# Kernel tuning notes

Measured on AMD Instinct MI355X. Metric: run time of the kernel, lower is better.

Reference implementation:

```python
import jax, jax.numpy as jnp
import numpy as np

N_NODES = 50000
N_EDGES = 800000
IN_DIM = 128
HID = 64
N_GRAPHS = 256


def gcn_conv(x, W, b, src, dst, num_nodes):
    """PyG GCNConv: add self-loops, sym norm D^-1/2 (A+I) D^-1/2, linear, bias."""
    h = x @ W  # [N, out]
    loop = jnp.arange(num_nodes)
    s = jnp.concatenate([src, loop])
    d = jnp.concatenate([dst, loop])
    ones = jnp.ones(d.shape, h.dtype)
    deg = jax.ops.segment_sum(ones, d, num_segments=num_nodes)
    dinv = jnp.where(deg > 0, jax.lax.rsqrt(deg), 0.0)
    norm = dinv[s] * dinv[d]  # [E+N]
    msg = h[s] * norm[:, None]  # gather + scale (memory bound)
    out = jax.ops.segment_sum(msg, d, num_segments=num_nodes)  # scatter-add
    return out + b


def setup_inputs() -> dict:
    key = jax.random.key(0)
    ks = jax.random.split(key, 8)
    x = jax.random.normal(ks[0], (N_NODES, IN_DIM), dtype=jnp.float32)
    edge_index = jax.random.randint(ks[1], (2, N_EDGES), 0, N_NODES, dtype=jnp.int64)
    batch = jnp.sort(jax.random.randint(ks[2], (N_NODES,), 0, N_GRAPHS, dtype=jnp.int64))
    W1 = jax.random.normal(ks[3], (IN_DIM, HID), dtype=jnp.float32) / np.sqrt(IN_DIM)
    b1 = jnp.zeros((HID,), jnp.float32)
    W2 = jax.random.normal(ks[4], (HID, HID), dtype=jnp.float32) / np.sqrt(HID)
    b2 = jnp.zeros((HID,), jnp.float32)
    Wl = jax.random.normal(ks[5], (HID, 1), dtype=jnp.float32) / np.sqrt(HID)
    bl = jnp.zeros((1,), jnp.float32)
    return {"x": x, "W1": W1, "b1": b1, "W2": W2, "b2": b2,
            "Wl": Wl, "bl": bl, "edge_index": edge_index, "batch": batch}


def reference(x, W1, b1, W2, b2, Wl, bl, edge_index, batch):
    n = x.shape[0]
    src, dst = edge_index[0], edge_index[1]
    h = jax.nn.relu(gcn_conv(x, W1, b1, src, dst, n))
    # dropout is identity in eval mode
    h = jax.nn.relu(gcn_conv(h, W2, b2, src, dst, n))
    ones = jnp.ones((n,), h.dtype)
    counts = jax.ops.segment_sum(ones, batch, num_segments=N_GRAPHS)
    pooled = jax.ops.segment_sum(h, batch, num_segments=N_GRAPHS)
    pooled = pooled / jnp.maximum(counts, 1.0)[:, None]  # global_mean_pool
    return (pooled @ Wl + bl).reshape(-1)  # [N_GRAPHS]
```

## Files before the change

kernel.cpp:

```cpp
#include <hip/hip_runtime.h>
#include <hip/hip_fp16.h>
#include <math.h>

__global__ void zero32(int* __restrict__ p, int n) {
    int i = blockIdx.x * blockDim.x + threadIdx.x;
    if (i < n) p[i] = 0;
}

__global__ void hist_rank(const int* __restrict__ dst, int* __restrict__ cnt,
                          unsigned short* __restrict__ rank, int E) {
    int e = blockIdx.x * blockDim.x + threadIdx.x;
    if (e < E) rank[e] = (unsigned short)atomicAdd(&cnt[dst[e]], 1);
}

__global__ __launch_bounds__(256) void scan1_dinv(const int* __restrict__ cnt,
                                                  int* __restrict__ excl,
                                                  int* __restrict__ sums,
                                                  float* __restrict__ dinv, int n) {
    int i = blockIdx.x * 256 + threadIdx.x;
    int v = (i < n) ? cnt[i] : 0;
    if (i < n) dinv[i] = rsqrtf((float)(v + 1));
    int lane = threadIdx.x & 63;
    int w = threadIdx.x >> 6;
    int s = v;
#pragma unroll
    for (int off = 1; off < 64; off <<= 1) {
        int t = __shfl_up(s, off, 64);
        if (lane >= off) s += t;
    }
    __shared__ int wsum[4];
    if (lane == 63) wsum[w] = s;
    __syncthreads();
    int woff = 0;
#pragma unroll
    for (int k = 0; k < 3; ++k) if (k < w) woff += wsum[k];
    int incl = s + woff;
    if (i < n) excl[i] = incl - v;
    if (threadIdx.x == 255) sums[blockIdx.x] = incl;
}

__global__ __launch_bounds__(256) void scan2(int* __restrict__ sums, int nb) {
    int t = threadIdx.x;
    int v = (t < nb) ? sums[t] : 0;
    int lane = t & 63;
    int w = t >> 6;
    int s = v;
#pragma unroll
    for (int off = 1; off < 64; off <<= 1) {
        int u = __shfl_up(s, off, 64);
        if (lane >= off) s += u;
    }
    __shared__ int wsum[4];
    if (lane == 63) wsum[w] = s;
    __syncthreads();
    int woff = 0;
#pragma unroll
    for (int k = 0; k < 3; ++k) if (k < w) woff += wsum[k];
    int incl = s + woff;
    if (t < nb) sums[t] = incl - v;
}

__global__ __launch_bounds__(256) void scan3(const int* __restrict__ excl,
                                             const int* __restrict__ sums,
                                             int* __restrict__ rowptr, int n, int E) {
    int i = blockIdx.x * 256 + threadIdx.x;
    if (i < n) rowptr[i] = excl[i] + sums[i >> 8];
    if (i == n) rowptr[n] = E;
}

__global__ void fill_place(const int* __restrict__ src, const int* __restrict__ dst,
                           const unsigned short* __restrict__ rank,
                           const int* __restrict__ rowptr,
                           unsigned short* __restrict__ col, int E, int n) {
    const int g    = blockIdx.x & 7;
    const int nblk = gridDim.x >> 3;
    const int bid  = blockIdx.x >> 3;
    const int lo = (int)(((long)g * n) >> 3);
    const int hi = (int)(((long)(g + 1) * n) >> 3);
    for (long e = (long)bid * blockDim.x + threadIdx.x; e < E;
         e += (long)nblk * blockDim.x) {
        int d = dst[e];
        if (d < lo || d >= hi) continue;
        col[rowptr[d] + rank[e]] = (unsigned short)src[e];
    }
}

#define RL(x, k) __int_as_float(__builtin_amdgcn_readlane(__float_as_int(x), (k)))

__device__ __forceinline__ float ldf(const float* p, long i) { return p[i]; }
__device__ __forceinline__ float ldf(const __half* p, long i) { return __half2float(p[i]); }
__device__ __forceinline__ void stf(float* p, long i, float v) { p[i] = v; }
__device__ __forceinline__ void stf(__half* p, long i, float v) { p[i] = __float2half(v); }

template <int K, typename XT, typename YT>
__global__ __launch_bounds__(256) void gemm_bcast_scaled(const XT* __restrict__ X,
                                                         const float* __restrict__ W,
                                                         const float* __restrict__ dinv,
                                                         YT* __restrict__ Y, int n) {
    const int lane = threadIdx.x & 63;
    const long wid = (((long)blockIdx.x * blockDim.x) + threadIdx.x) >> 6;
    const long nw  = ((long)gridDim.x * blockDim.x) >> 6;

    float wr[K];
#pragma unroll
    for (int k = 0; k < K; ++k) wr[k] = W[k * 64 + lane];
#pragma unroll
    for (int k = 0; k < K; ++k) asm volatile("" : "+v"(wr[k]));

    long r0 = wid;
    if (r0 >= n) return;
    float xa0 = ldf(X, r0 * K + lane);
    float xb0 = 0.f;
    if constexpr (K > 64) xb0 = ldf(X, r0 * K + 64 + lane);
    float dv0 = dinv[r0];

    long r1 = r0 + nw;
    bool h1 = r1 < n;
    long rc1 = h1 ? r1 : r0;
    float xa1 = ldf(X, rc1 * K + lane);
    float xb1 = 0.f;
    if constexpr (K > 64) xb1 = ldf(X, rc1 * K + 64 + lane);
    float dv1 = dinv[rc1];

    while (true) {
        long r2 = r1 + nw;
        bool h2 = h1 && (r2 < n);
        long rc2 = h2 ? r2 : r0;
        float xa2 = ldf(X, rc2 * K + lane);
        float xb2 = 0.f;
        if constexpr (K > 64) xb2 = ldf(X, rc2 * K + 64 + lane);
        float dv2 = dinv[rc2];

        float a0 = 0.f, a1 = 0.f, a2 = 0.f, a3 = 0.f;
#pragma unroll
        for (int k = 0; k < 64; k += 4) {
            a0 = fmaf(RL(xa0, k + 0), wr[k + 0], a0);
            a1 = fmaf(RL(xa0, k + 1), wr[k + 1], a1);
            a2 = fmaf(RL(xa0, k + 2), wr[k + 2], a2);
            a3 = fmaf(RL(xa0, k + 3), wr[k + 3], a3);
        }
        if constexpr (K > 64) {
#pragma unroll
            for (int k = 0; k < 64; k += 4) {
                a0 = fmaf(RL(xb0, k + 0), wr[64 + k + 0], a0);
                a1 = fmaf(RL(xb0, k + 1), wr[64 + k + 1], a1);
                a2 = fmaf(RL(xb0, k + 2), wr[64 + k + 2], a2);
                a3 = fmaf(RL(xb0, k + 3), wr[64 + k + 3], a3);
            }
        }
        stf(Y, r0 * 64 + lane, dv0 * ((a0 + a1) + (a2 + a3)));
        if (!h1) break;
        r0 = r1; xa0 = xa1; xb0 = xb1; dv0 = dv1;
        r1 = r2; h1 = h2; xa1 = xa2; xb1 = xb2; dv1 = dv2;
    }
}

#define HG(idx) ldf(Hp, (long)(idx) * 64 + j)
template <typename HT>
__device__ __forceinline__ void agg2(const HT* __restrict__ Hp,
                                     const int* __restrict__ rowptr,
                                     const unsigned short* __restrict__ col,
                                     long vA, long vB, int j, bool hasB,
                                     float& sumA, float& sumB) {
    float a0 = HG(vA), a1 = 0.f, a2 = 0.f, a3 = 0.f;
    float b0 = 0.f, b1 = 0.f, b2 = 0.f, b3 = 0.f;
    int pA = rowptr[vA], pA1 = rowptr[vA + 1];
    int pB = 0, pB1 = 0;
    if (hasB) { b0 = HG(vB); pB = rowptr[vB]; pB1 = rowptr[vB + 1]; }
    if ((pA & 1) && pA < pA1) { a1 += HG(col[pA]); ++pA; }
    if ((pB & 1) && pB < pB1) { b1 += HG(col[pB]); ++pB; }
    unsigned int cA01 = *(const unsigned int*)(col + pA);
    unsigned int cA23 = *(const unsigned int*)(col + pA + 2);
    unsigned int cB01 = *(const unsigned int*)(col + pB);
    unsigned int cB23 = *(const unsigned int*)(col + pB + 2);
    while (pA + 4 <= pA1 && pB + 4 <= pB1) {
        unsigned int nA01 = *(const unsigned int*)(col + pA + 4);
        unsigned int nA23 = *(const unsigned int*)(col + pA + 6);
        unsigned int nB01 = *(const unsigned int*)(col + pB + 4);
        unsigned int nB23 = *(const unsigned int*)(col + pB + 6);
        float hA0 = HG(cA01 & 0xFFFFu);
        float hA1 = HG(cA01 >> 16);
        float hA2 = HG(cA23 & 0xFFFFu);
        float hA3 = HG(cA23 >> 16);
        float hB0 = HG(cB01 & 0xFFFFu);
        float hB1 = HG(cB01 >> 16);
        float hB2 = HG(cB23 & 0xFFFFu);
        float hB3 = HG(cB23 >> 16);
        a0 += hA0; a1 += hA1; a2 += hA2; a3 += hA3;
        b0 += hB0; b1 += hB1; b2 += hB2; b3 += hB3;
        cA01 = nA01; cA23 = nA23; cB01 = nB01; cB23 = nB23;
        pA += 4; pB += 4;
    }
    for (; pA + 4 <= pA1; pA += 4) {
        float h0 = HG(cA01 & 0xFFFFu);
        float h1 = HG(cA01 >> 16);
        float h2 = HG(cA23 & 0xFFFFu);
        float h3 = HG(cA23 >> 16);
        a0 += h0; a1 += h1; a2 += h2; a3 += h3;
        cA01 = *(const unsigned int*)(col + pA + 4);
        cA23 = *(const unsigned int*)(col + pA + 6);
    }
    for (; pA < pA1; ++pA) a1 += HG(col[pA]);
    for (; pB + 4 <= pB1; pB += 4) {
        float h0 = HG(cB01 & 0xFFFFu);
        float h1 = HG(cB01 >> 16);
        float h2 = HG(cB23 & 0xFFFFu);
        float h3 = HG(cB23 >> 16);
        b0 += h0; b1 += h1; b2 += h2; b3 += h3;
        cB01 = *(const unsigned int*)(col + pB + 4);
        cB23 = *(const unsigned int*)(col + pB + 6);
    }
    for (; pB < pB1; ++pB) b1 += HG(col[pB]);
    sumA = (a0 + a1) + (a2 + a3);
    sumB = (b0 + b1) + (b2 + b3);
}

__global__ __launch_bounds__(256) void agg_relu(const __half* __restrict__ Hp,
                                                const int* __restrict__ rowptr,
                                                const unsigned short* __restrict__ col,
                                                const float* __restrict__ dinv,
                                                const float* __restrict__ bias,
                                                float* __restrict__ out, int n) {
    const int j = threadIdx.x & 63;
    const long wid = (((long)blockIdx.x * blockDim.x) + threadIdx.x) >> 6;
    const long NW  = ((long)gridDim.x * blockDim.x) >> 6;
    const float bj = bias[j];
    for (long vA = wid; vA < n; vA += 2 * NW) {
        long vB = vA + NW;
        bool hasB = vB < n;
        float sA, sB;
        agg2(Hp, rowptr, col, vA, vB, j, hasB, sA, sB);
        float diA = dinv[vA];
        float diB = hasB ? dinv[vB] : 0.f;
        out[vA * 64 + j] = fmaxf(diA * sA + bj, 0.f);
        if (hasB) out[vB * 64 + j] = fmaxf(diB * sB + bj, 0.f);
    }
}

__global__ __launch_bounds__(256) void agg_pool(const float* __restrict__ Hp,
                                                const int* __restrict__ rowptr,
                                                const unsigned short* __restrict__ col,
                                                const float* __restrict__ dinv,
                                                const float* __restrict__ bias,
                                                const float* __restrict__ Wl,
                                                const int* __restrict__ batch,
                                                float* __restrict__ part,
                                                float* __restrict__ partc, int n) {
    __shared__ float lp[256];
    __shared__ float lc[256];
    lp[threadIdx.x] = 0.f;
    lc[threadIdx.x] = 0.f;
    __syncthreads();
    const int j  = threadIdx.x & 63;
    const int wv = threadIdx.x >> 6;
    const float bj  = bias[j];
    const float wlj = Wl[j];
    const long wid = (long)blockIdx.x * 4 + wv;
    const long NW  = (long)gridDim.x * 4;
    for (long vA = wid; vA < n; vA += 2 * NW) {
        long vB = vA + NW;
        bool hasB = vB < n;
        float sA, sB;
        agg2(Hp, rowptr, col, vA, vB, j, hasB, sA, sB);
        float diA = dinv[vA];
        float diB = hasB ? dinv[vB] : 0.f;
        float valA = fmaxf(diA * sA + bj, 0.f) * wlj;
        float valB = fmaxf(diB * sB + bj, 0.f) * wlj;
#pragma unroll
        for (int off = 32; off > 0; off >>= 1) {
            valA += __shfl_down(valA, off, 64);
            valB += __shfl_down(valB, off, 64);
        }
        if (j == 0) {
            atomicAdd(&lp[batch[vA]], valA);
            atomicAdd(&lc[batch[vA]], 1.0f);
            if (hasB) {
                atomicAdd(&lp[batch[vB]], valB);
                atomicAdd(&lc[batch[vB]], 1.0f);
            }
        }
    }
    __syncthreads();
    long o = (long)blockIdx.x * 256 + threadIdx.x;
    part[o]  = lp[threadIdx.x];
    partc[o] = lc[threadIdx.x];
}

__global__ __launch_bounds__(256) void pool_final(const float* __restrict__ part,
                                                  const float* __restrict__ partc,
                                                  const float* __restrict__ bl,
                                                  float* __restrict__ out, int nblk) {
    int g = blockIdx.x;
    int t = threadIdx.x;
    float s = 0.f, c = 0.f;
    for (int b = t; b < nblk; b += 256) {
        s += part[(long)b * 256 + g];
        c += partc[(long)b * 256 + g];
    }
    __shared__ float sp[256];
    __shared__ float sc[256];
    sp[t] = s;
    sc[t] = c;
    __syncthreads();
    for (int off = 128; off > 0; off >>= 1) {
        if (t < off) { sp[t] += sp[t + off]; sc[t] += sc[t + off]; }
        __syncthreads();
    }
    if (t == 0) out[g] = sp[0] / fmaxf(sc[0], 1.0f) + bl[0];
}

extern "C" void kernel_launch(void* const* d_in, const int* in_sizes, int n_in,
                              void* d_out, int out_size, void* d_ws, size_t ws_size,
                              hipStream_t stream) {
    const float* x  = (const float*)d_in[0];
    const float* W1 = (const float*)d_in[1];
    const float* b1 = (const float*)d_in[2];
    const float* W2 = (const float*)d_in[3];
    const float* b2 = (const float*)d_in[4];
    const float* Wl = (const float*)d_in[5];
    const float* bl = (const float*)d_in[6];
    const int* edge_index = (const int*)d_in[7];
    const int* batch      = (const int*)d_in[8];

    const int n = in_sizes[0] / 128;
    const int E = in_sizes[7] / 2;
    const int G = out_size;
    const int* src = edge_index;
    const int* dst = edge_index + E;

    char* ws = (char*)d_ws;
    size_t off = 0;
    auto alloc = [&](size_t bytes) { void* p = ws + off; off = (off + bytes + 255) & ~(size_t)255; return p; };
    int*            cntv   = (int*)           alloc((size_t)n * 4);
    float*          dinv   = (float*)         alloc((size_t)n * 4);
    int*            rowptr = (int*)           alloc((size_t)(n + 1) * 4);
    int*            excl   = (int*)           alloc((size_t)n * 4);
    int*            sums   = (int*)           alloc((size_t)256 * 4);
    unsigned short* rank   = (unsigned short*)alloc((size_t)E * 2);
    unsigned short* col    = (unsigned short*)alloc((size_t)E * 2 + 64);
    __half*         bufA   = (__half*)        alloc((size_t)n * 64 * 2);
    float*          bufC   = (float*)         alloc((size_t)n * 64 * 4);
    float*          bufB   = (float*)         alloc((size_t)n * 64 * 4);
    const int PBLK = 2048;
    float*          part   = (float*)         alloc((size_t)PBLK * 256 * 4);
    float*          partc  = (float*)         alloc((size_t)PBLK * 256 * 4);

    const int T = 256;
    const int nchunks = (n + 255) / 256;
    zero32<<<(n + T - 1) / T, T, 0, stream>>>(cntv, n);
    hist_rank<<<(E + T - 1) / T, T, 0, stream>>>(dst, cntv, rank, E);
    scan1_dinv<<<nchunks, T, 0, stream>>>(cntv, excl, sums, dinv, n);
    scan2<<<1, T, 0, stream>>>(sums, nchunks);
    scan3<<<(n + 1 + T - 1) / T, T, 0, stream>>>(excl, sums, rowptr, n, E);
    fill_place<<<1024, T, 0, stream>>>(src, dst, rank, rowptr, col, E, n);

    gemm_bcast_scaled<128><<<768, T, 0, stream>>>(x, W1, dinv, bufA, n);
    agg_relu<<<2048, T, 0, stream>>>(bufA, rowptr, col, dinv, b1, bufC, n);
    gemm_bcast_scaled<64><<<768, T, 0, stream>>>(bufC, W2, dinv, bufB, n);
    agg_pool<<<PBLK, T, 0, stream>>>(bufB, rowptr, col, dinv, b2, Wl, batch, part, partc, n);
    pool_final<<<G, T, 0, stream>>>(part, partc, bl, (float*)d_out, PBLK);
}
```

Measured before the change: 178.4 us.

## Fuse CSR build stages into one cooperative kernel with grid syncs

```diff
diff --git a/kernel.cpp b/kernel.cpp
--- a/kernel.cpp
+++ b/kernel.cpp
@@ -1,87 +1,96 @@
 #include <hip/hip_runtime.h>
 #include <hip/hip_fp16.h>
+#include <hip/hip_cooperative_groups.h>
 #include <math.h>
 
-__global__ void zero32(int* __restrict__ p, int n) {
-    int i = blockIdx.x * blockDim.x + threadIdx.x;
-    if (i < n) p[i] = 0;
-}
-
-__global__ void hist_rank(const int* __restrict__ dst, int* __restrict__ cnt,
-                          unsigned short* __restrict__ rank, int E) {
-    int e = blockIdx.x * blockDim.x + threadIdx.x;
-    if (e < E) rank[e] = (unsigned short)atomicAdd(&cnt[dst[e]], 1);
-}
-
-__global__ __launch_bounds__(256) void scan1_dinv(const int* __restrict__ cnt,
-                                                  int* __restrict__ excl,
-                                                  int* __restrict__ sums,
-                                                  float* __restrict__ dinv, int n) {
-    int i = blockIdx.x * 256 + threadIdx.x;
-    int v = (i < n) ? cnt[i] : 0;
-    if (i < n) dinv[i] = rsqrtf((float)(v + 1));
-    int lane = threadIdx.x & 63;
-    int w = threadIdx.x >> 6;
-    int s = v;
-#pragma unroll
-    for (int off = 1; off < 64; off <<= 1) {
-        int t = __shfl_up(s, off, 64);
-        if (lane >= off) s += t;
-    }
+namespace cg = cooperative_groups;
+
+__global__ __launch_bounds__(256) void build_csr(const int* __restrict__ src,
+                                                 const int* __restrict__ dst,
+                                                 int* __restrict__ cnt,
+                                                 unsigned short* __restrict__ rank,
+                                                 int* __restrict__ excl,
+                                                 int* __restrict__ sums,
+                                                 float* __restrict__ dinv,
+                                                 int* __restrict__ rowptr,
+                                                 unsigned short* __restrict__ col,
+                                                 int n, int E, int nchunks) {
+    cg::grid_group grid = cg::this_grid();
     __shared__ int wsum[4];
-    if (lane == 63) wsum[w] = s;
-    __syncthreads();
-    int woff = 0;
-#pragma unroll
-    for (int k = 0; k < 3; ++k) if (k < w) woff += wsum[k];
-    int incl = s + woff;
-    if (i < n) excl[i] = incl - v;
-    if (threadIdx.x == 255) sums[blockIdx.x] = incl;
-}
-
-__global__ __launch_bounds__(256) void scan2(int* __restrict__ sums, int nb) {
-    int t = threadIdx.x;
-    int v = (t < nb) ? sums[t] : 0;
-    int lane = t & 63;
-    int w = t >> 6;
-    int s = v;
-#pragma unroll
-    for (int off = 1; off < 64; off <<= 1) {
-        int u = __shfl_up(s, off, 64);
-        if (lane >= off) s += u;
-    }
-    __shared__ int wsum[4];
-    if (lane == 63) wsum[w] = s;
-    __syncthreads();
-    int woff = 0;
-#pragma unroll
-    for (int k = 0; k < 3; ++k) if (k < w) woff += wsum[k];
-    int incl = s + woff;
-    if (t < nb) sums[t] = incl - v;
-}
-
-__global__ __launch_bounds__(256) void scan3(const int* __restrict__ excl,
-                                             const int* __restrict__ sums,
-                                             int* __restrict__ rowptr, int n, int E) {
-    int i = blockIdx.x * 256 + threadIdx.x;
-    if (i < n) rowptr[i] = excl[i] + sums[i >> 8];
-    if (i == n) rowptr[n] = E;
-}
-
-__global__ void fill_place(const int* __restrict__ src, const int* __restrict__ dst,
-                           const unsigned short* __restrict__ rank,
-                           const int* __restrict__ rowptr,
-                           unsigned short* __restrict__ col, int E, int n) {
-    const int g    = blockIdx.x & 7;
-    const int nblk = gridDim.x >> 3;
-    const int bid  = blockIdx.x >> 3;
-    const int lo = (int)(((long)g * n) >> 3);
-    const int hi = (int)(((long)(g + 1) * n) >> 3);
-    for (long e = (long)bid * blockDim.x + threadIdx.x; e < E;
-         e += (long)nblk * blockDim.x) {
-        int d = dst[e];
-        if (d < lo || d >= hi) continue;
-        col[rowptr[d] + rank[e]] = (unsigned short)src[e];
+    const long gt = (long)blockIdx.x * 256 + threadIdx.x;
+    const long GS = (long)gridDim.x * 256;
+    const int lane = threadIdx.x & 63;
+    const int w    = threadIdx.x >> 6;
+
+    for (long i = gt; i < n; i += GS) cnt[i] = 0;
+    grid.sync();
+
+    for (long e = gt; e < E; e += GS)
+        rank[e] = (unsigned short)atomicAdd(&cnt[dst[e]], 1);
+    grid.sync();
+
+    for (int c = blockIdx.x; c < nchunks; c += gridDim.x) {
+        int i = c * 256 + threadIdx.x;
+        int v = (i < n) ? cnt[i] : 0;
+        int s = v;
+#pragma unroll
+        for (int off = 1; off < 64; off <<= 1) {
+            int t = __shfl_up(s, off, 64);
+            if (lane >= off) s += t;
+        }
+        if (lane == 63) wsum[w] = s;
+        __syncthreads();
+        int woff = 0;
+#pragma unroll
+        for (int k = 0; k < 3; ++k) if (k < w) woff += wsum[k];
+        int incl = s + woff;
+        if (i < n) excl[i] = incl - v;
+        if (threadIdx.x == 255) sums[c] = incl;
+        __syncthreads();
+    }
+    grid.sync();
+
+    if (blockIdx.x == 0) {
+        int t = threadIdx.x;
+        int v = (t < nchunks) ? sums[t] : 0;
+        int s = v;
+#pragma unroll
+        for (int off = 1; off < 64; off <<= 1) {
+            int u = __shfl_up(s, off, 64);
+            if (lane >= off) s += u;
+        }
+        if (lane == 63) wsum[w] = s;
+        __syncthreads();
+        int woff = 0;
+#pragma unroll
+        for (int k = 0; k < 3; ++k) if (k < w) woff += wsum[k];
+        int incl = s + woff;
+        if (t < nchunks) sums[t] = incl - v;
+    }
+    grid.sync();
+
+    for (long i = gt; i <= n; i += GS) {
+        if (i < n) {
+            rowptr[i] = excl[i] + sums[i >> 8];
+            dinv[i] = rsqrtf((float)(cnt[i] + 1));
+        } else if (i == n) {
+            rowptr[n] = E;
+        }
+    }
+    grid.sync();
+
+    {
+        const int g    = blockIdx.x & 7;
+        const int nblk = gridDim.x >> 3;
+        const int bid  = blockIdx.x >> 3;
+        const int lo = (int)(((long)g * n) >> 3);
+        const int hi = (int)(((long)(g + 1) * n) >> 3);
+        for (long e = (long)bid * 256 + threadIdx.x; e < E;
+             e += (long)nblk * 256) {
+            int d = dst[e];
+            if (d < lo || d >= hi) continue;
+            col[rowptr[d] + rank[e]] = (unsigned short)src[e];
+        }
     }
 }
 
@@ -322,8 +331,8 @@
     const int* edge_index = (const int*)d_in[7];
     const int* batch      = (const int*)d_in[8];
 
-    const int n = in_sizes[0] / 128;
-    const int E = in_sizes[7] / 2;
+    int n = in_sizes[0] / 128;
+    int E = in_sizes[7] / 2;
     const int G = out_size;
     const int* src = edge_index;
     const int* dst = edge_index + E;
@@ -346,13 +355,15 @@
     float*          partc  = (float*)         alloc((size_t)PBLK * 256 * 4);
 
     const int T = 256;
-    const int nchunks = (n + 255) / 256;
-    zero32<<<(n + T - 1) / T, T, 0, stream>>>(cntv, n);
-    hist_rank<<<(E + T - 1) / T, T, 0, stream>>>(dst, cntv, rank, E);
-    scan1_dinv<<<nchunks, T, 0, stream>>>(cntv, excl, sums, dinv, n);
-    scan2<<<1, T, 0, stream>>>(sums, nchunks);
-    scan3<<<(n + 1 + T - 1) / T, T, 0, stream>>>(excl, sums, rowptr, n, E);
-    fill_place<<<1024, T, 0, stream>>>(src, dst, rank, rowptr, col, E, n);
+    int nchunks = (n + 255) / 256;
+
+    {
+        void* args[] = {(void*)&src, (void*)&dst, (void*)&cntv, (void*)&rank,
+                        (void*)&excl, (void*)&sums, (void*)&dinv, (void*)&rowptr,
+                        (void*)&col, (void*)&n, (void*)&E, (void*)&nchunks};
+        hipLaunchCooperativeKernel((const void*)build_csr, dim3(1024), dim3(T),
+                                   args, 0, stream);
+    }
 
     gemm_bcast_scaled<128><<<768, T, 0, stream>>>(x, W1, dinv, bufA, n);
     agg_relu<<<2048, T, 0, stream>>>(bufA, rowptr, col, dinv, b1, bufC, n);
```

Result: slower. 651.7 us (+265.3%).
